# Performance work log

Hardware: AMD Instinct MI355X
Metric: run time of the kernel (lower is better)

## Reference

```python
import jax, jax.numpy as jnp
import numpy as np

N_NODES = 100000
N_EDGES = 1600000
NFEAT, NHID, NCLASS, NL = 128, 64, 40, 6


def setup_inputs() -> dict:
    key = jax.random.key(0)
    ks = jax.random.split(key, 12)
    x = jax.random.normal(ks[0], (N_NODES, NFEAT), dtype=jnp.float32)
    edge_row = jax.random.randint(ks[1], (N_EDGES,), 0, N_NODES)
    edge_col = jax.random.randint(ks[2], (N_EDGES,), 0, N_NODES)
    # positive values mimicking a degree-normalized adjacency
    edge_val = jax.random.uniform(ks[3], (N_EDGES,), dtype=jnp.float32) / 16.0
    s1 = 1.0 / np.sqrt(NFEAT)
    sh = 1.0 / np.sqrt(NHID)
    W1 = jax.random.uniform(ks[4], (NFEAT, NHID), minval=-s1, maxval=s1, dtype=jnp.float32)
    b1 = jax.random.uniform(ks[5], (NHID,), minval=-s1, maxval=s1, dtype=jnp.float32)
    Wm = jax.random.uniform(ks[6], (NL, NHID, NHID), minval=-sh, maxval=sh, dtype=jnp.float32)
    bm = jax.random.uniform(ks[7], (NL, NHID), minval=-sh, maxval=sh, dtype=jnp.float32)
    W2 = jax.random.uniform(ks[8], (NHID, NCLASS), minval=-sh, maxval=sh, dtype=jnp.float32)
    b2 = jax.random.uniform(ks[9], (NCLASS,), minval=-sh, maxval=sh, dtype=jnp.float32)
    return {"x": x, "edge_row": edge_row, "edge_col": edge_col, "edge_val": edge_val,
            "W1": W1, "b1": b1, "Wm": Wm, "bm": bm, "W2": W2, "b2": b2}


def _gconv(h, row, col, val, W, b):
    # GraphConvolution: support = h @ W ; out = spmm(adj, support) + b
    support = h @ W                       # [N, out]
    msgs = val[:, None] * support[col]    # [E, out] gather
    agg = jax.ops.segment_sum(msgs, row, num_segments=h.shape[0])  # scatter-add
    return agg + b


def reference(x, edge_row, edge_col, edge_val, W1, b1, Wm, bm, W2, b2):
    # gc1: relu (dropout is identity in eval mode)
    h1 = jax.nn.relu(_gconv(x, edge_row, edge_col, edge_val, W1, b1))
    # first middle layer (module index 2): relu, no residual
    h2 = jax.nn.relu(_gconv(h1, edge_row, edge_col, edge_val, Wm[0], bm[0]))
    prev2, prev = h1, h2
    # remaining middle layers: relu + residual to two layers back
    for k in range(1, NL):
        h = jax.nn.relu(_gconv(prev, edge_row, edge_col, edge_val, Wm[k], bm[k])) + prev2
        prev2, prev = prev, h
    out = _gconv(prev, edge_row, edge_col, edge_val, W2, b2)  # gc2, no relu
    return jax.nn.log_softmax(out, axis=1)
```

## Files before the change

### kernel.cpp

```cpp
#include <hip/hip_runtime.h>
#include <hip/hip_bf16.h>
#include <math.h>

#define N_NODES 100000
#define N_EDGES 1600000
#define NFEAT 128
#define NHID  64
#define NCLASS 40
#define NL 6

#define NBUK 256
#define RPB  391
#define EPP  (N_EDGES / NBUK)
#define EP_PAD 256

typedef __attribute__((ext_vector_type(8))) short short8;
typedef __attribute__((ext_vector_type(4))) float floatx4;

__device__ __forceinline__ float bfbits(unsigned short u) {
  return __uint_as_float((unsigned int)u << 16);
}
__device__ __forceinline__ short f2bs(float f) {
  __hip_bfloat16 h = __float2bfloat16(f);
  return *reinterpret_cast<short*>(&h);
}

__global__ __launch_bounds__(256) void p0_hist_k(const int* __restrict__ row,
                                                 int* __restrict__ h2d) {
  __shared__ int h[NBUK];
  const int i = blockIdx.x, t = threadIdx.x;
  h[t] = 0;
  __syncthreads();
  const int e0 = i * EPP, e1 = e0 + EPP;
  for (int e = e0 + t; e < e1; e += 256) atomicAdd(&h[row[e] / RPB], 1);
  __syncthreads();
  h2d[i * NBUK + t] = h[t];
}

__global__ __launch_bounds__(256) void k1_scanb_k(int* __restrict__ h2d,
                                                  int* __restrict__ btot) {
  __shared__ int sd[256];
  const int b = blockIdx.x, t = threadIdx.x;
  int v = h2d[t * NBUK + b];
  sd[t] = v;
  __syncthreads();
  for (int off = 1; off < 256; off <<= 1) {
    int a = (t >= off) ? sd[t - off] : 0;
    __syncthreads();
    sd[t] += a;
    __syncthreads();
  }
  h2d[t * NBUK + b] = sd[t] - v;
  if (t == 255) btot[b] = sd[255];
}

__global__ __launch_bounds__(256) void k2_scanbase_k(const int* __restrict__ btot,
                                                     int* __restrict__ bbase,
                                                     int2* __restrict__ ep) {
  __shared__ int sd[256];
  const int t = threadIdx.x;
  int v = btot[t];
  sd[t] = v;
  __syncthreads();
  for (int off = 1; off < 256; off <<= 1) {
    int a = (t >= off) ? sd[t - off] : 0;
    __syncthreads();
    sd[t] += a;
    __syncthreads();
  }
  bbase[t] = sd[t] - v;
  if (t == 255) bbase[256] = sd[255];
  if (t < EP_PAD) ep[N_EDGES + t] = make_int2(0, 0);
}

__global__ __launch_bounds__(256) void p2_part_k(
    const int* __restrict__ row, const int* __restrict__ col,
    const float* __restrict__ val, const int* __restrict__ h2d,
    const int* __restrict__ bbase, int2* __restrict__ pcv,
    unsigned short* __restrict__ plr) {
  __shared__ int cur[NBUK];
  const int i = blockIdx.x, t = threadIdx.x;
  cur[t] = bbase[t] + h2d[i * NBUK + t];
  __syncthreads();
  const int e0 = i * EPP, e1 = e0 + EPP;
  for (int e = e0 + t; e < e1; e += 256) {
    int r = row[e];
    int b = r / RPB;
    int p = atomicAdd(&cur[b], 1);
    pcv[p] = make_int2(col[e], __float_as_int(val[e]));
    plr[p] = (unsigned short)(r - b * RPB);
  }
}

__global__ __launch_bounds__(256) void p3_fine_k(const int2* __restrict__ pcv,
                                                 const unsigned short* __restrict__ plr,
                                                 const int* __restrict__ bbase,
                                                 int* __restrict__ rp,
                                                 int2* __restrict__ ep) {
  __shared__ int cnt[RPB];
  __shared__ int cur[RPB];
  const int b = blockIdx.x, t = threadIdx.x;
  const int ebeg = bbase[b], eend = bbase[b + 1];
  const int r0 = b * RPB;
  const int nloc = min(RPB, N_NODES - r0);

  for (int i = t; i < RPB; i += 256) cnt[i] = 0;
  __syncthreads();
  for (int j = ebeg + t; j < eend; j += 256) atomicAdd(&cnt[plr[j]], 1);
  __syncthreads();

  if (t < 64) {
    const int base_ = t * 7;
    int v[7], s = 0;
#pragma unroll
    for (int k = 0; k < 7; ++k) {
      int idx = base_ + k;
      v[k] = (idx < RPB) ? cnt[idx] : 0;
      s += v[k];
    }
    int incl = s;
#pragma unroll
    for (int off = 1; off < 64; off <<= 1) {
      int y = __shfl_up(incl, off);
      if (t >= off) incl += y;
    }
    int run = incl - s;
#pragma unroll
    for (int k = 0; k < 7; ++k) {
      int idx = base_ + k;
      if (idx < RPB) cnt[idx] = run;
      run += v[k];
    }
  }
  __syncthreads();

  for (int i = t; i < nloc; i += 256) {
    rp[r0 + i] = ebeg + cnt[i];
    cur[i] = cnt[i];
  }
  if (b == 0 && t == 0) rp[N_NODES] = N_EDGES;
  __syncthreads();

  for (int j = ebeg + t; j < eend; j += 256) {
    int lr = plr[j];
    int p = atomicAdd(&cur[lr], 1);
    ep[ebeg + p] = pcv[j];
  }
}

template <int K, int COLS>
__global__ __launch_bounds__(256) void gemm_mfma(const float* __restrict__ H,
                                                 const float* __restrict__ W,
                                                 __hip_bfloat16* __restrict__ S) {
  constexpr int NK = K / 32;
  const int lane = threadIdx.x & 63;
  const int quad = lane >> 4;
  const int m = lane & 15;

  short8 bf[4][NK];
#pragma unroll
  for (int t = 0; t < 4; ++t) {
    const int cc = t * 16 + m;
#pragma unroll
    for (int h = 0; h < NK; ++h) {
#pragma unroll
      for (int j = 0; j < 8; ++j) {
        const int kk = h * 32 + quad * 8 + j;
        bf[t][h][j] = (COLS == 64 || cc < COLS) ? f2bs(W[kk * COLS + cc]) : (short)0;
      }
    }
  }

  const int r0 = blockIdx.x * 64 + (threadIdx.x >> 6) * 16;
  if (r0 >= N_NODES) return;
  const int arow = min(r0 + m, N_NODES - 1);

  short8 af[NK];
#pragma unroll
  for (int h = 0; h < NK; ++h) {
    const float* hp = H + (size_t)arow * K + h * 32 + quad * 8;
    float4 p0 = *(const float4*)hp;
    float4 p1 = *(const float4*)(hp + 4);
    af[h][0] = f2bs(p0.x); af[h][1] = f2bs(p0.y);
    af[h][2] = f2bs(p0.z); af[h][3] = f2bs(p0.w);
    af[h][4] = f2bs(p1.x); af[h][5] = f2bs(p1.y);
    af[h][6] = f2bs(p1.z); af[h][7] = f2bs(p1.w);
  }

  floatx4 acc[4];
#pragma unroll
  for (int t = 0; t < 4; ++t) {
    acc[t] = {0.0f, 0.0f, 0.0f, 0.0f};
#pragma unroll
    for (int h = 0; h < NK; ++h)
      acc[t] = __builtin_amdgcn_mfma_f32_16x16x32_bf16(af[h], bf[t][h], acc[t], 0, 0, 0);
  }

  unsigned short* Sp = (unsigned short*)S;
#pragma unroll
  for (int t = 0; t < 4; ++t) {
#pragma unroll
    for (int r = 0; r < 4; ++r) {
      const int row = r0 + quad * 4 + r;
      if (row < N_NODES)
        Sp[(size_t)row * 64 + t * 16 + m] = (unsigned short)f2bs(acc[t][r]);
    }
  }
}

template <bool RES>
__global__ __launch_bounds__(256) void spmm16_k(
    const __hip_bfloat16* __restrict__ Sin, const int2* __restrict__ ep,
    const int* __restrict__ rp, const float* __restrict__ bias,
    const float* __restrict__ res, float* __restrict__ Hout) {
  const int lane = threadIdx.x & 63;
  const int g = lane >> 4;
  const int i16 = lane & 15;
  const int gl = g & 1;
  const int pair = blockIdx.x * 4 + (threadIdx.x >> 6);
  const int nodeA = pair * 2;
  const int sA = rp[nodeA], sB = rp[nodeA + 1], eB = rp[nodeA + 2];
  const bool isB = (g >= 2);
  const int myNode = nodeA + (isB ? 1 : 0);
  const int myEnd = isB ? eB : sB;
  const int iters = (max(sB - sA, eB - sB) + 7) >> 3;

  const unsigned short* S = (const unsigned short*)Sin;
  const int foff = i16 * 4;

  float a0 = 0.0f, a1 = 0.0f, a2 = 0.0f, a3 = 0.0f;
  int e = (isB ? sB : sA) + gl * 2;
  for (int it = 0; it < iters; ++it, e += 8) {
    const int o0 = e, o1 = e + 1, o2 = e + 4, o3 = e + 5;
    int2 q0 = ep[o0];
    int2 q1 = ep[o1];
    int2 q2 = ep[o2];
    int2 q3 = ep[o3];
    float v0 = (o0 < myEnd) ? __int_as_float(q0.y) : 0.0f;
    float v1 = (o1 < myEnd) ? __int_as_float(q1.y) : 0.0f;
    float v2 = (o2 < myEnd) ? __int_as_float(q2.y) : 0.0f;
    float v3 = (o3 < myEnd) ? __int_as_float(q3.y) : 0.0f;
    ushort4 s0 = *(const ushort4*)(S + ((q0.x << 6) + foff));
    ushort4 s1 = *(const ushort4*)(S + ((q1.x << 6) + foff));
    ushort4 s2 = *(const ushort4*)(S + ((q2.x << 6) + foff));
    ushort4 s3 = *(const ushort4*)(S + ((q3.x << 6) + foff));
    a0 = fmaf(v0, bfbits(s0.x), a0); a1 = fmaf(v0, bfbits(s0.y), a1);
    a2 = fmaf(v0, bfbits(s0.z), a2); a3 = fmaf(v0, bfbits(s0.w), a3);
    a0 = fmaf(v1, bfbits(s1.x), a0); a1 = fmaf(v1, bfbits(s1.y), a1);
    a2 = fmaf(v1, bfbits(s1.z), a2); a3 = fmaf(v1, bfbits(s1.w), a3);
    a0 = fmaf(v2, bfbits(s2.x), a0); a1 = fmaf(v2, bfbits(s2.y), a1);
    a2 = fmaf(v2, bfbits(s2.z), a2); a3 = fmaf(v2, bfbits(s2.w), a3);
    a0 = fmaf(v3, bfbits(s3.x), a0); a1 = fmaf(v3, bfbits(s3.y), a1);
    a2 = fmaf(v3, bfbits(s3.z), a2); a3 = fmaf(v3, bfbits(s3.w), a3);
  }

  a0 += __shfl_xor(a0, 16);
  a1 += __shfl_xor(a1, 16);
  a2 += __shfl_xor(a2, 16);
  a3 += __shfl_xor(a3, 16);

  if ((g & 1) == 0) {
    float4 b4 = ((const float4*)bias)[i16];
    float h0 = fmaxf(a0 + b4.x, 0.0f);
    float h1 = fmaxf(a1 + b4.y, 0.0f);
    float h2 = fmaxf(a2 + b4.z, 0.0f);
    float h3 = fmaxf(a3 + b4.w, 0.0f);
    if (RES) {
      float4 r4 = ((const float4*)res)[myNode * 16 + i16];
      h0 += r4.x; h1 += r4.y; h2 += r4.z; h3 += r4.w;
    }
    ((float4*)Hout)[myNode * 16 + i16] = make_float4(h0, h1, h2, h3);
  }
}

__global__ __launch_bounds__(256) void spmm_final_k(
    const __hip_bfloat16* __restrict__ Sin, const int2* __restrict__ ep,
    const int* __restrict__ rp, const float* __restrict__ b2,
    float* __restrict__ out) {
  const int lane = threadIdx.x & 63;
  const int g = lane >> 4;
  const int i16 = lane & 15;
  const int gl = g & 1;
  const int pair = blockIdx.x * 4 + (threadIdx.x >> 6);
  const int nodeA = pair * 2;
  const int sA = rp[nodeA], sB = rp[nodeA + 1], eB = rp[nodeA + 2];
  const bool isB = (g >= 2);
  const int myNode = nodeA + (isB ? 1 : 0);
  const int myEnd = isB ? eB : sB;
  const int iters = (max(sB - sA, eB - sB) + 7) >> 3;

  const unsigned short* S = (const unsigned short*)Sin;
  const int foff = i16 * 4;

  float a0 = 0.0f, a1 = 0.0f, a2 = 0.0f, a3 = 0.0f;
  int e = (isB ? sB : sA) + gl * 2;
  for (int it = 0; it < iters; ++it, e += 8) {
    const int o0 = e, o1 = e + 1, o2 = e + 4, o3 = e + 5;
    int2 q0 = ep[o0];
    int2 q1 = ep[o1];
    int2 q2 = ep[o2];
    int2 q3 = ep[o3];
    float v0 = (o0 < myEnd) ? __int_as_float(q0.y) : 0.0f;
    float v1 = (o1 < myEnd) ? __int_as_float(q1.y) : 0.0f;
    float v2 = (o2 < myEnd) ? __int_as_float(q2.y) : 0.0f;
    float v3 = (o3 < myEnd) ? __int_as_float(q3.y) : 0.0f;
    ushort4 s0 = *(const ushort4*)(S + ((q0.x << 6) + foff));
    ushort4 s1 = *(const ushort4*)(S + ((q1.x << 6) + foff));
    ushort4 s2 = *(const ushort4*)(S + ((q2.x << 6) + foff));
    ushort4 s3 = *(const ushort4*)(S + ((q3.x << 6) + foff));
    a0 = fmaf(v0, bfbits(s0.x), a0); a1 = fmaf(v0, bfbits(s0.y), a1);
    a2 = fmaf(v0, bfbits(s0.z), a2); a3 = fmaf(v0, bfbits(s0.w), a3);
    a0 = fmaf(v1, bfbits(s1.x), a0); a1 = fmaf(v1, bfbits(s1.y), a1);
    a2 = fmaf(v1, bfbits(s1.z), a2); a3 = fmaf(v1, bfbits(s1.w), a3);
    a0 = fmaf(v2, bfbits(s2.x), a0); a1 = fmaf(v2, bfbits(s2.y), a1);
    a2 = fmaf(v2, bfbits(s2.z), a2); a3 = fmaf(v2, bfbits(s2.w), a3);
    a0 = fmaf(v3, bfbits(s3.x), a0); a1 = fmaf(v3, bfbits(s3.y), a1);
    a2 = fmaf(v3, bfbits(s3.z), a2); a3 = fmaf(v3, bfbits(s3.w), a3);
  }
  a0 += __shfl_xor(a0, 16);
  a1 += __shfl_xor(a1, 16);
  a2 += __shfl_xor(a2, 16);
  a3 += __shfl_xor(a3, 16);

  const bool valid = (i16 < 10);
  float l0 = -INFINITY, l1 = -INFINITY, l2 = -INFINITY, l3 = -INFINITY;
  if (valid) {
    float4 b4 = ((const float4*)b2)[i16];
    l0 = a0 + b4.x; l1 = a1 + b4.y; l2 = a2 + b4.z; l3 = a3 + b4.w;
  }
  float mx = fmaxf(fmaxf(l0, l1), fmaxf(l2, l3));
#pragma unroll
  for (int off = 1; off < 16; off <<= 1) mx = fmaxf(mx, __shfl_xor(mx, off));
  float sum = valid ? (expf(l0 - mx) + expf(l1 - mx) + expf(l2 - mx) + expf(l3 - mx)) : 0.0f;
#pragma unroll
  for (int off = 1; off < 16; off <<= 1) sum += __shfl_xor(sum, off);
  if (((g & 1) == 0) && valid) {
    float lg = logf(sum);
    ((float4*)out)[myNode * 10 + i16] =
        make_float4(l0 - mx - lg, l1 - mx - lg, l2 - mx - lg, l3 - mx - lg);
  }
}

extern "C" void kernel_launch(void* const* d_in, const int* in_sizes, int n_in,
                              void* d_out, int out_size, void* d_ws, size_t ws_size,
                              hipStream_t stream) {
  const float* x    = (const float*)d_in[0];
  const int*   erow = (const int*)d_in[1];
  const int*   ecol = (const int*)d_in[2];
  const float* eval = (const float*)d_in[3];
  const float* W1   = (const float*)d_in[4];
  const float* b1   = (const float*)d_in[5];
  const float* Wm   = (const float*)d_in[6];
  const float* bm   = (const float*)d_in[7];
  const float* W2   = (const float*)d_in[8];
  const float* b2   = (const float*)d_in[9];
  float* out = (float*)d_out;

  char* ws = (char*)d_ws;
  size_t off = 0;
  auto alloc = [&](size_t bytes) {
    void* p = ws + off;
    off = (off + bytes + 255) & ~(size_t)255;
    return p;
  };
  int*  rp    = (int*)alloc((N_NODES + 1) * sizeof(int));
  int*  h2d   = (int*)alloc((size_t)NBUK * NBUK * sizeof(int));
  int*  btot  = (int*)alloc(NBUK * sizeof(int));
  int*  bbase = (int*)alloc((NBUK + 1) * sizeof(int));
  int2* ep    = (int2*)alloc((size_t)(N_EDGES + EP_PAD) * sizeof(int2));
  char* U     = (char*)alloc((size_t)N_EDGES * sizeof(int2) +
                             (((size_t)N_EDGES * sizeof(unsigned short) + 255) & ~(size_t)255));
  int2* pcv = (int2*)U;
  unsigned short* plr = (unsigned short*)(U + (size_t)N_EDGES * sizeof(int2));
  __hip_bfloat16* S = (__hip_bfloat16*)U;
  float* H0 = (float*)alloc((size_t)N_NODES * 64 * sizeof(float));
  float* H1 = (float*)alloc((size_t)N_NODES * 64 * sizeof(float));

  const int SPMM_GRID = N_NODES / 8;
  const int GEMM_GRID = (N_NODES + 63) / 64;

  p0_hist_k<<<NBUK, 256, 0, stream>>>(erow, h2d);
  k1_scanb_k<<<NBUK, 256, 0, stream>>>(h2d, btot);
  k2_scanbase_k<<<1, 256, 0, stream>>>(btot, bbase, ep);
  p2_part_k<<<NBUK, 256, 0, stream>>>(erow, ecol, eval, h2d, bbase, pcv, plr);
  p3_fine_k<<<NBUK, 256, 0, stream>>>(pcv, plr, bbase, rp, ep);

  gemm_mfma<128, 64><<<GEMM_GRID, 256, 0, stream>>>(x, W1, S);
  spmm16_k<false><<<SPMM_GRID, 256, 0, stream>>>(S, ep, rp, b1, nullptr, H0);

  gemm_mfma<64, 64><<<GEMM_GRID, 256, 0, stream>>>(H0, Wm, S);
  spmm16_k<false><<<SPMM_GRID, 256, 0, stream>>>(S, ep, rp, bm, nullptr, H1);

  float* prev2 = H0;
  float* prev  = H1;
  for (int k = 1; k < NL; ++k) {
    gemm_mfma<64, 64><<<GEMM_GRID, 256, 0, stream>>>(prev, Wm + (size_t)k * 4096, S);
    spmm16_k<true><<<SPMM_GRID, 256, 0, stream>>>(S, ep, rp, bm + k * 64, prev2, prev2);
    float* t = prev2; prev2 = prev; prev = t;
  }

  gemm_mfma<64, 40><<<GEMM_GRID, 256, 0, stream>>>(prev, W2, S);
  spmm_final_k<<<SPMM_GRID, 256, 0, stream>>>(S, ep, rp, b2, out);
}
```

Baseline: 554.4 us.

## Emit bf16 hidden copy from SpMM for GEMM input, persistent GEMM grid

Each SpMM epilogue now also writes a bf16 copy of the hidden activations. The next GEMM reads that copy instead of re-reading and converting the fp32 matrix, which halves its input traffic. fp32 stores are skipped when the tensor is no longer needed as a residual. The GEMMs become grid-stride kernels over 16-row tiles with a fixed 512-block grid, so the weight fragments are loaded once per wave rather than once per tile. The cost is an extra bf16 write in every SpMM, and the layer loop is unrolled by hand to track which fp32 buffers are still live.

```diff
diff --git a/kernel.cpp b/kernel.cpp
--- a/kernel.cpp
+++ b/kernel.cpp
@@ -13,6 +13,7 @@
 #define RPB  391
 #define EPP  (N_EDGES / NBUK)
 #define EP_PAD 256
+#define NTILES (N_NODES / 16)
 
 typedef __attribute__((ext_vector_type(8))) short short8;
 typedef __attribute__((ext_vector_type(4))) float floatx4;
@@ -148,71 +149,95 @@
   }
 }
 
-template <int K, int COLS>
-__global__ __launch_bounds__(256) void gemm_mfma(const float* __restrict__ H,
-                                                 const float* __restrict__ W,
-                                                 __hip_bfloat16* __restrict__ S) {
-  constexpr int NK = K / 32;
+__global__ __launch_bounds__(256) void gemm_l1(const float* __restrict__ X,
+                                               const float* __restrict__ W,
+                                               unsigned short* __restrict__ S) {
   const int lane = threadIdx.x & 63;
   const int quad = lane >> 4;
   const int m = lane & 15;
 
-  short8 bf[4][NK];
+  short8 bf[4][4];
+#pragma unroll
+  for (int t = 0; t < 4; ++t)
+#pragma unroll
+    for (int h = 0; h < 4; ++h)
+#pragma unroll
+      for (int j = 0; j < 8; ++j)
+        bf[t][h][j] = f2bs(W[(h * 32 + quad * 8 + j) * 64 + t * 16 + m]);
+
+  const int wid = blockIdx.x * 4 + (threadIdx.x >> 6);
+  for (int tile = wid; tile < NTILES; tile += gridDim.x * 4) {
+    const int r0 = tile * 16;
+    const float* xr = X + (size_t)(r0 + m) * 128;
+    short8 af[4];
+#pragma unroll
+    for (int h = 0; h < 4; ++h) {
+      const float* p = xr + h * 32 + quad * 8;
+      float4 a = *(const float4*)p;
+      float4 b = *(const float4*)(p + 4);
+      af[h][0] = f2bs(a.x); af[h][1] = f2bs(a.y);
+      af[h][2] = f2bs(a.z); af[h][3] = f2bs(a.w);
+      af[h][4] = f2bs(b.x); af[h][5] = f2bs(b.y);
+      af[h][6] = f2bs(b.z); af[h][7] = f2bs(b.w);
+    }
+#pragma unroll
+    for (int t = 0; t < 4; ++t) {
+      floatx4 acc = {0.0f, 0.0f, 0.0f, 0.0f};
+#pragma unroll
+      for (int h = 0; h < 4; ++h)
+        acc = __builtin_amdgcn_mfma_f32_16x16x32_bf16(af[h], bf[t][h], acc, 0, 0, 0);
+#pragma unroll
+      for (int r = 0; r < 4; ++r)
+        S[(size_t)(r0 + quad * 4 + r) * 64 + t * 16 + m] = (unsigned short)f2bs(acc[r]);
+    }
+  }
+}
+
+template <int COLS>
+__global__ __launch_bounds__(256) void gemm_bf(const unsigned short* __restrict__ Hb,
+                                               const float* __restrict__ W,
+                                               unsigned short* __restrict__ S) {
+  const int lane = threadIdx.x & 63;
+  const int quad = lane >> 4;
+  const int m = lane & 15;
+
+  short8 bf[4][2];
 #pragma unroll
   for (int t = 0; t < 4; ++t) {
     const int cc = t * 16 + m;
 #pragma unroll
-    for (int h = 0; h < NK; ++h) {
-#pragma unroll
-      for (int j = 0; j < 8; ++j) {
-        const int kk = h * 32 + quad * 8 + j;
-        bf[t][h][j] = (COLS == 64 || cc < COLS) ? f2bs(W[kk * COLS + cc]) : (short)0;
-      }
-    }
-  }
-
-  const int r0 = blockIdx.x * 64 + (threadIdx.x >> 6) * 16;
-  if (r0 >= N_NODES) return;
-  const int arow = min(r0 + m, N_NODES - 1);
-
-  short8 af[NK];
-#pragma unroll
-  for (int h = 0; h < NK; ++h) {
-    const float* hp = H + (size_t)arow * K + h * 32 + quad * 8;
-    float4 p0 = *(const float4*)hp;
-    float4 p1 = *(const float4*)(hp + 4);
-    af[h][0] = f2bs(p0.x); af[h][1] = f2bs(p0.y);
-    af[h][2] = f2bs(p0.z); af[h][3] = f2bs(p0.w);
-    af[h][4] = f2bs(p1.x); af[h][5] = f2bs(p1.y);
-    af[h][6] = f2bs(p1.z); af[h][7] = f2bs(p1.w);
-  }
-
-  floatx4 acc[4];
-#pragma unroll
-  for (int t = 0; t < 4; ++t) {
-    acc[t] = {0.0f, 0.0f, 0.0f, 0.0f};
-#pragma unroll
-    for (int h = 0; h < NK; ++h)
-      acc[t] = __builtin_amdgcn_mfma_f32_16x16x32_bf16(af[h], bf[t][h], acc[t], 0, 0, 0);
-  }
-
-  unsigned short* Sp = (unsigned short*)S;
-#pragma unroll
-  for (int t = 0; t < 4; ++t) {
-#pragma unroll
-    for (int r = 0; r < 4; ++r) {
-      const int row = r0 + quad * 4 + r;
-      if (row < N_NODES)
-        Sp[(size_t)row * 64 + t * 16 + m] = (unsigned short)f2bs(acc[t][r]);
-    }
-  }
-}
-
-template <bool RES>
+    for (int h = 0; h < 2; ++h)
+#pragma unroll
+      for (int j = 0; j < 8; ++j)
+        bf[t][h][j] = (COLS == 64 || cc < COLS)
+                          ? f2bs(W[(h * 32 + quad * 8 + j) * COLS + cc])
+                          : (short)0;
+  }
+
+  const int wid = blockIdx.x * 4 + (threadIdx.x >> 6);
+  for (int tile = wid; tile < NTILES; tile += gridDim.x * 4) {
+    const int r0 = tile * 16;
+    const unsigned short* hr = Hb + (size_t)(r0 + m) * 64 + quad * 8;
+    short8 af0 = *(const short8*)hr;
+    short8 af1 = *(const short8*)(hr + 32);
+#pragma unroll
+    for (int t = 0; t < 4; ++t) {
+      floatx4 acc = {0.0f, 0.0f, 0.0f, 0.0f};
+      acc = __builtin_amdgcn_mfma_f32_16x16x32_bf16(af0, bf[t][0], acc, 0, 0, 0);
+      acc = __builtin_amdgcn_mfma_f32_16x16x32_bf16(af1, bf[t][1], acc, 0, 0, 0);
+#pragma unroll
+      for (int r = 0; r < 4; ++r)
+        S[(size_t)(r0 + quad * 4 + r) * 64 + t * 16 + m] = (unsigned short)f2bs(acc[r]);
+    }
+  }
+}
+
+template <bool RES, bool STOREF>
 __global__ __launch_bounds__(256) void spmm16_k(
-    const __hip_bfloat16* __restrict__ Sin, const int2* __restrict__ ep,
+    const unsigned short* __restrict__ S, const int2* __restrict__ ep,
     const int* __restrict__ rp, const float* __restrict__ bias,
-    const float* __restrict__ res, float* __restrict__ Hout) {
+    const float* __restrict__ res, float* __restrict__ Hout,
+    unsigned short* __restrict__ Hbout) {
   const int lane = threadIdx.x & 63;
   const int g = lane >> 4;
   const int i16 = lane & 15;
@@ -225,7 +250,6 @@
   const int myEnd = isB ? eB : sB;
   const int iters = (max(sB - sA, eB - sB) + 7) >> 3;
 
-  const unsigned short* S = (const unsigned short*)Sin;
   const int foff = i16 * 4;
 
   float a0 = 0.0f, a1 = 0.0f, a2 = 0.0f, a3 = 0.0f;
@@ -269,12 +293,19 @@
       float4 r4 = ((const float4*)res)[myNode * 16 + i16];
       h0 += r4.x; h1 += r4.y; h2 += r4.z; h3 += r4.w;
     }
-    ((float4*)Hout)[myNode * 16 + i16] = make_float4(h0, h1, h2, h3);
+    if (STOREF)
+      ((float4*)Hout)[myNode * 16 + i16] = make_float4(h0, h1, h2, h3);
+    ushort4 hb;
+    hb.x = (unsigned short)f2bs(h0);
+    hb.y = (unsigned short)f2bs(h1);
+    hb.z = (unsigned short)f2bs(h2);
+    hb.w = (unsigned short)f2bs(h3);
+    ((ushort4*)Hbout)[myNode * 16 + i16] = hb;
   }
 }
 
 __global__ __launch_bounds__(256) void spmm_final_k(
-    const __hip_bfloat16* __restrict__ Sin, const int2* __restrict__ ep,
+    const unsigned short* __restrict__ S, const int2* __restrict__ ep,
     const int* __restrict__ rp, const float* __restrict__ b2,
     float* __restrict__ out) {
   const int lane = threadIdx.x & 63;
@@ -289,7 +320,6 @@
   const int myEnd = isB ? eB : sB;
   const int iters = (max(sB - sA, eB - sB) + 7) >> 3;
 
-  const unsigned short* S = (const unsigned short*)Sin;
   const int foff = i16 * 4;
 
   float a0 = 0.0f, a1 = 0.0f, a2 = 0.0f, a3 = 0.0f;
@@ -372,12 +402,13 @@
                              (((size_t)N_EDGES * sizeof(unsigned short) + 255) & ~(size_t)255));
   int2* pcv = (int2*)U;
   unsigned short* plr = (unsigned short*)(U + (size_t)N_EDGES * sizeof(int2));
-  __hip_bfloat16* S = (__hip_bfloat16*)U;
-  float* H0 = (float*)alloc((size_t)N_NODES * 64 * sizeof(float));
-  float* H1 = (float*)alloc((size_t)N_NODES * 64 * sizeof(float));
+  unsigned short* S = (unsigned short*)U;
+  float* F0 = (float*)alloc((size_t)N_NODES * 64 * sizeof(float));
+  float* F1 = (float*)alloc((size_t)N_NODES * 64 * sizeof(float));
+  unsigned short* Hb = (unsigned short*)alloc((size_t)N_NODES * 64 * sizeof(unsigned short));
 
   const int SPMM_GRID = N_NODES / 8;
-  const int GEMM_GRID = (N_NODES + 63) / 64;
+  const int GEMM_GRID = 512;
 
   p0_hist_k<<<NBUK, 256, 0, stream>>>(erow, h2d);
   k1_scanb_k<<<NBUK, 256, 0, stream>>>(h2d, btot);
@@ -385,20 +416,27 @@
   p2_part_k<<<NBUK, 256, 0, stream>>>(erow, ecol, eval, h2d, bbase, pcv, plr);
   p3_fine_k<<<NBUK, 256, 0, stream>>>(pcv, plr, bbase, rp, ep);
 
-  gemm_mfma<128, 64><<<GEMM_GRID, 256, 0, stream>>>(x, W1, S);
-  spmm16_k<false><<<SPMM_GRID, 256, 0, stream>>>(S, ep, rp, b1, nullptr, H0);
-
-  gemm_mfma<64, 64><<<GEMM_GRID, 256, 0, stream>>>(H0, Wm, S);
-  spmm16_k<false><<<SPMM_GRID, 256, 0, stream>>>(S, ep, rp, bm, nullptr, H1);
-
-  float* prev2 = H0;
-  float* prev  = H1;
-  for (int k = 1; k < NL; ++k) {
-    gemm_mfma<64, 64><<<GEMM_GRID, 256, 0, stream>>>(prev, Wm + (size_t)k * 4096, S);
-    spmm16_k<true><<<SPMM_GRID, 256, 0, stream>>>(S, ep, rp, bm + k * 64, prev2, prev2);
-    float* t = prev2; prev2 = prev; prev = t;
-  }
-
-  gemm_mfma<64, 40><<<GEMM_GRID, 256, 0, stream>>>(prev, W2, S);
+  gemm_l1<<<GEMM_GRID, 256, 0, stream>>>(x, W1, S);
+  spmm16_k<false, true><<<SPMM_GRID, 256, 0, stream>>>(S, ep, rp, b1, nullptr, F0, Hb);
+
+  gemm_bf<64><<<GEMM_GRID, 256, 0, stream>>>(Hb, Wm, S);
+  spmm16_k<false, true><<<SPMM_GRID, 256, 0, stream>>>(S, ep, rp, bm, nullptr, F1, Hb);
+
+  gemm_bf<64><<<GEMM_GRID, 256, 0, stream>>>(Hb, Wm + 1 * 4096, S);
+  spmm16_k<true, true><<<SPMM_GRID, 256, 0, stream>>>(S, ep, rp, bm + 1 * 64, F0, F0, Hb);
+
+  gemm_bf<64><<<GEMM_GRID, 256, 0, stream>>>(Hb, Wm + 2 * 4096, S);
+  spmm16_k<true, true><<<SPMM_GRID, 256, 0, stream>>>(S, ep, rp, bm + 2 * 64, F1, F1, Hb);
+
+  gemm_bf<64><<<GEMM_GRID, 256, 0, stream>>>(Hb, Wm + 3 * 4096, S);
+  spmm16_k<true, true><<<SPMM_GRID, 256, 0, stream>>>(S, ep, rp, bm + 3 * 64, F0, F0, Hb);
+
+  gemm_bf<64><<<GEMM_GRID, 256, 0, stream>>>(Hb, Wm + 4 * 4096, S);
+  spmm16_k<true, false><<<SPMM_GRID, 256, 0, stream>>>(S, ep, rp, bm + 4 * 64, F1, nullptr, Hb);
+
+  gemm_bf<64><<<GEMM_GRID, 256, 0, stream>>>(Hb, Wm + 5 * 4096, S);
+  spmm16_k<true, false><<<SPMM_GRID, 256, 0, stream>>>(S, ep, rp, bm + 5 * 64, F0, nullptr, Hb);
+
+  gemm_bf<40><<<GEMM_GRID, 256, 0, stream>>>(Hb, W2, S);
   spmm_final_k<<<SPMM_GRID, 256, 0, stream>>>(S, ep, rp, b2, out);
 }
```

Result: slower. 565.5 us (+2.0%).
